# Performance work log

Measured on AMD Instinct MI355X. Metric: run time of the kernel, lower is better.

The kernel has to match this reference:

```python
import jax, jax.numpy as jnp
import numpy as np

N = 8192      # nodes
E = 8192      # target edges
H = 256       # in_channels == hidden_channels (required by module structure)
OUT = 1
ADJ_P = 0.004 # ~33 avg degree


def _linear_params(key, din, dout):
    kw, kb = jax.random.split(key)
    s = 1.0 / np.sqrt(din)
    w = jax.random.uniform(kw, (din, dout), jnp.float32, -s, s)
    b = jax.random.uniform(kb, (dout,), jnp.float32, -s, s)
    return w, b


def setup_inputs() -> dict:
    key = jax.random.key(0)
    ks = jax.random.split(key, 10)
    x = jax.random.normal(ks[0], (N, H), jnp.float32)
    # binary adjacency (symmetric not required by the math)
    adj = (jax.random.uniform(ks[1], (N, N)) < ADJ_P).astype(jnp.float32)
    tar_ei = jax.random.randint(ks[2], (2, E), 0, N)
    xlin_w, xlin_b = _linear_params(ks[3], H, H)
    xcnlin_w, xcnlin_b = _linear_params(ks[4], H, H)
    xijlini_w, xijlini_b = _linear_params(ks[5], H, H)
    xijlinj_w, xijlinj_b = _linear_params(ks[6], H, H)
    xijfinal_w, xijfinal_b = _linear_params(ks[7], H, H)
    xslin_w, xslin_b = _linear_params(ks[8], H, OUT)
    beta = jnp.ones((1,), jnp.float32)
    return {
        'x': x, 'adj': adj, 'tar_ei': tar_ei,
        'xlin_w': xlin_w, 'xlin_b': xlin_b,
        'xcnlin_w': xcnlin_w, 'xcnlin_b': xcnlin_b,
        'xijlini_w': xijlini_w, 'xijlini_b': xijlini_b,
        'xijlinj_w': xijlinj_w, 'xijlinj_b': xijlinj_b,
        'xijfinal_w': xijfinal_w, 'xijfinal_b': xijfinal_b,
        'xslin_w': xslin_w, 'xslin_b': xslin_b,
        'beta': beta, 'boolen': 1,
    }


def reference(x, adj, tar_ei, xlin_w, xlin_b, xcnlin_w, xcnlin_b,
              xijlini_w, xijlini_b, xijlinj_w, xijlinj_b,
              xijfinal_w, xijfinal_b, xslin_w, xslin_b, beta, boolen):
    src, dst = tar_ei[0], tar_ei[1]
    xi = x[src]                       # [E,H]
    xj = x[dst]                       # [E,H]
    x2 = x + (x @ xlin_w + xlin_b)    # x = x + xlin(x)
    # adjoverlap: common-neighbor indicator per target edge = A[i] AND A[j]
    cn = adj[src] * adj[dst]          # [E,N] binary mask
    xcn = cn @ x2                     # spmm_add(cn, x) -> [E,H]
    xij = jax.nn.relu((xi @ xijlini_w + xijlini_b) + (xj @ xijlinj_w + xijlinj_b))
    xij = xij @ xijfinal_w + xijfinal_b
    xs = (xcn @ xcnlin_w + xcnlin_b) * beta + xij
    # NOTE: source's `xs.relu()` result is discarded (not in-place) -> no relu
    xs = xs @ xslin_w + xslin_b       # [E,OUT]
    sign = 1.0 if boolen else -1.0
    return -jax.nn.log_sigmoid(sign * xs)
```

## Files before the change

kernel.cpp:

```cpp
#include <hip/hip_runtime.h>

#define Nn 8192
#define Ee 8192
#define Hh 256
#define MASK_W 128
#define RQ 16
#define NPQ 512

typedef unsigned long long u64;
typedef float nf4 __attribute__((ext_vector_type(4)));

__global__ void __launch_bounds__(256)
pre_kernel(const float* __restrict__ Wc, const float* __restrict__ Wf,
           const float* __restrict__ Wx, const float* __restrict__ v_,
           const float* __restrict__ bc, const float* __restrict__ bf_,
           const float* __restrict__ bx, const float* __restrict__ bs,
           const float* __restrict__ beta, const int* __restrict__ boolen,
           float* __restrict__ w2, float* __restrict__ g,
           float* __restrict__ consts) {
    __shared__ float sv[Hh];
    __shared__ float su[Hh];
    __shared__ float r1[Hh], r2[Hh], r3[Hh];
    const int tid = threadIdx.x;
    sv[tid] = v_[tid];
    __syncthreads();

    const float4* wc4 = reinterpret_cast<const float4*>(Wc + (size_t)tid * Hh);
    const float4* wf4 = reinterpret_cast<const float4*>(Wf + (size_t)tid * Hh);
    const float4* sv4 = reinterpret_cast<const float4*>(sv);
    float a = 0.f, b = 0.f;
#pragma unroll 8
    for (int j = 0; j < Hh / 4; ++j) {
        const float4 w = wc4[j];
        const float4 f = wf4[j];
        const float4 s = sv4[j];
        a = fmaf(w.x, s.x, fmaf(w.y, s.y, fmaf(w.z, s.z, fmaf(w.w, s.w, a))));
        b = fmaf(f.x, s.x, fmaf(f.y, s.y, fmaf(f.z, s.z, fmaf(f.w, s.w, b))));
    }
    su[tid] = a;
    w2[tid] = b;
    __syncthreads();

    const float4* wx4 = reinterpret_cast<const float4*>(Wx + (size_t)tid * Hh);
    const float4* su4 = reinterpret_cast<const float4*>(su);
    float c = a;
#pragma unroll 8
    for (int j = 0; j < Hh / 4; ++j) {
        const float4 w = wx4[j];
        const float4 uu = su4[j];
        c = fmaf(w.x, uu.x, fmaf(w.y, uu.y, fmaf(w.z, uu.z, fmaf(w.w, uu.w, c))));
    }
    g[tid] = c;

    r1[tid] = bc[tid] * sv[tid];
    r2[tid] = bf_[tid] * sv[tid];
    r3[tid] = bx[tid] * a;
    __syncthreads();
    for (int s = 128; s > 0; s >>= 1) {
        if (tid < s) { r1[tid] += r1[tid + s]; r2[tid] += r2[tid + s]; r3[tid] += r3[tid + s]; }
        __syncthreads();
    }
    if (tid == 0) {
        const float be = beta[0];
        consts[0] = r3[0];
        consts[1] = be * r1[0] + r2[0] + bs[0];
        consts[2] = (boolen[0] != 0) ? 1.f : -1.f;
        consts[3] = be;
    }
}

__global__ void __launch_bounds__(256)
fusedA_kernel(const float* __restrict__ adj, u64* __restrict__ mask,
              const float* __restrict__ x,
              const float* __restrict__ Wi, const float* __restrict__ Wj,
              const float* __restrict__ bi, const float* __restrict__ bj,
              const float* __restrict__ g, const float* __restrict__ consts,
              float* __restrict__ P, float* __restrict__ Q,
              float* __restrict__ t) {
    __shared__ float xs[RQ][Hh];
    const int tid = threadIdx.x;

    if (blockIdx.x >= NPQ) {
        const int wave_id = (blockIdx.x - NPQ) * 4 + (tid >> 6);
        const int lane = tid & 63;
        const int row  = wave_id >> 1;
        const int half = wave_id & 1;
        const nf4* src = reinterpret_cast<const nf4*>(
            adj + (size_t)row * Nn + half * 4096);

        u64 myword = 0;
#pragma unroll
        for (int i = 0; i < 16; ++i) {
            const nf4 v = __builtin_nontemporal_load(src + i * 64 + lane);
            unsigned int nib = 0;
            nib |= (v.x != 0.f) ? 1u : 0u;
            nib |= (v.y != 0.f) ? 2u : 0u;
            nib |= (v.z != 0.f) ? 4u : 0u;
            nib |= (v.w != 0.f) ? 8u : 0u;
            const unsigned int t1 = __shfl_xor(nib, 1);
            const unsigned int by = nib | (t1 << 4);
            const unsigned int t2 = __shfl_xor(by, 2);
            const unsigned int h16 = by | (t2 << 8);
            const unsigned int t4 = __shfl_xor(h16, 4);
            const unsigned int w32 = h16 | (t4 << 16);
            const unsigned int t8 = __shfl_xor(w32, 8);
            const u64 w64 = (u64)w32 | ((u64)t8 << 32);
            const u64 got = __shfl(w64, (lane & 3) << 4);
            if ((lane >> 2) == i) myword = got;
        }
        mask[(size_t)row * MASK_W + half * 64 + lane] = myword;
        return;
    }

    const int base = blockIdx.x * RQ;
    {
        const float4* xv = reinterpret_cast<const float4*>(x + (size_t)base * Hh);
        float4* xd = reinterpret_cast<float4*>(&xs[0][0]);
#pragma unroll
        for (int i = tid; i < 1024; i += 256) xd[i] = xv[i];
    }
    __syncthreads();

    {
        const int wave = tid >> 6;
        const int lane = tid & 63;
        const float c0 = consts[0];
#pragma unroll
        for (int r0 = 0; r0 < 4; ++r0) {
            const int r = wave * 4 + r0;
            float s = 0.f;
#pragma unroll
            for (int i = 0; i < 4; ++i) {
                const int c = lane * 4 + i;
                s = fmaf(xs[r][c], g[c], s);
            }
            for (int off = 32; off > 0; off >>= 1) s += __shfl_down(s, off);
            if (lane == 0) t[base + r] = s + c0;
        }
    }

    float accP[RQ], accQ[RQ];
    const float fbi = bi[tid], fbj = bj[tid];
#pragma unroll
    for (int r = 0; r < RQ; ++r) { accP[r] = fbi; accQ[r] = fbj; }

#pragma unroll 4
    for (int k = 0; k < Hh; ++k) {
        const float wiv = Wi[k * Hh + tid];
        const float wjv = Wj[k * Hh + tid];
#pragma unroll
        for (int r = 0; r < RQ; ++r) {
            accP[r] = fmaf(xs[r][k], wiv, accP[r]);
            accQ[r] = fmaf(xs[r][k], wjv, accQ[r]);
        }
    }
#pragma unroll
    for (int r = 0; r < RQ; ++r) {
        P[(size_t)(base + r) * Hh + tid] = accP[r];
        Q[(size_t)(base + r) * Hh + tid] = accQ[r];
    }
}

__global__ void edge_kernel(const u64* __restrict__ mask, const int* __restrict__ tei,
                            const float* __restrict__ P, const float* __restrict__ Q,
                            const float* __restrict__ w2, const float* __restrict__ t,
                            const float* __restrict__ consts, float* __restrict__ out) {
    const int e = blockIdx.x;
    const int tid = threadIdx.x;
    const int src = tei[e];
    const int dst = tei[Ee + e];

    __shared__ u64 ms[MASK_W];
    __shared__ u64 md[MASK_W];
    if (tid < MASK_W) ms[tid] = mask[(size_t)src * MASK_W + tid];
    else              md[tid - MASK_W] = mask[(size_t)dst * MASK_W + (tid - MASK_W)];
    __syncthreads();

    float accA = 0.f;
    if (tid < MASK_W) {
        u64 m = ms[tid] & md[tid];
        while (m) {
            const int b = __builtin_ctzll(m);
            accA += t[tid * 64 + b];
            m &= m - 1;
        }
    }
    const float r = P[(size_t)src * Hh + tid] + Q[(size_t)dst * Hh + tid];
    float accB = (r > 0.f) ? r * w2[tid] : 0.f;

    for (int off = 32; off > 0; off >>= 1) {
        accA += __shfl_down(accA, off);
        accB += __shfl_down(accB, off);
    }
    __shared__ float wA[4], wB[4];
    const int wave = tid >> 6;
    if ((tid & 63) == 0) { wA[wave] = accA; wB[wave] = accB; }
    __syncthreads();
    if (tid == 0) {
        const float sA = wA[0] + wA[1] + wA[2] + wA[3];
        const float sB = wB[0] + wB[1] + wB[2] + wB[3];
        const float be = consts[3];
        const float sgn = consts[2];
        const float s = be * sA + sB + consts[1];
        const float m = -sgn * s;
        const float res = fmaxf(m, 0.f) + log1pf(expf(-fabsf(m)));
        out[e] = res;
    }
}

extern "C" void kernel_launch(void* const* d_in, const int* in_sizes, int n_in,
                              void* d_out, int out_size, void* d_ws, size_t ws_size,
                              hipStream_t stream) {
    const float* x     = (const float*)d_in[0];
    const float* adj   = (const float*)d_in[1];
    const int*   tei   = (const int*)d_in[2];
    const float* Wx    = (const float*)d_in[3];
    const float* bx    = (const float*)d_in[4];
    const float* Wc    = (const float*)d_in[5];
    const float* bc    = (const float*)d_in[6];
    const float* Wi    = (const float*)d_in[7];
    const float* bi    = (const float*)d_in[8];
    const float* Wj    = (const float*)d_in[9];
    const float* bj    = (const float*)d_in[10];
    const float* Wf    = (const float*)d_in[11];
    const float* bf_   = (const float*)d_in[12];
    const float* v_    = (const float*)d_in[13];
    const float* bs    = (const float*)d_in[14];
    const float* beta  = (const float*)d_in[15];
    const int*   booln = (const int*)d_in[16];
    float* out = (float*)d_out;

    float* w2     = (float*)d_ws;
    float* g      = w2 + 256;
    float* consts = g + 256;
    float* t      = consts + 8;
    float* P      = t + 8192;
    float* Q      = P + (size_t)Nn * Hh;
    u64*   mask   = (u64*)(Q + (size_t)Nn * Hh);

    pre_kernel<<<1, 256, 0, stream>>>(Wc, Wf, Wx, v_, bc, bf_, bx, bs, beta,
                                      booln, w2, g, consts);
    fusedA_kernel<<<NPQ + (Nn * 2) / 4, 256, 0, stream>>>(adj, mask, x, Wi, Wj,
                                                          bi, bj, g, consts,
                                                          P, Q, t);
    edge_kernel<<<Ee, 256, 0, stream>>>(mask, tei, P, Q, w2, t, consts, out);
}
```

Baseline: 447.7 us.

## Fold single-block precompute kernel into fusedA by recomputing per block

Removes the separate one-block pre_kernel launch. Each P/Q block of fusedA now recomputes the weight-vector products g and c0 redundantly into shared memory, and block 0 alone writes w2 and consts for the edge kernel. This drops one kernel launch and the serial dependency on a single-block kernel. In exchange, each of the 512 P/Q blocks does two extra 256x256 matrix-vector products, reading Wc and Wx, before its main work.

```diff
diff --git a/kernel.cpp b/kernel.cpp
--- a/kernel.cpp
+++ b/kernel.cpp
@@ -11,73 +11,20 @@
 typedef float nf4 __attribute__((ext_vector_type(4)));
 
 __global__ void __launch_bounds__(256)
-pre_kernel(const float* __restrict__ Wc, const float* __restrict__ Wf,
-           const float* __restrict__ Wx, const float* __restrict__ v_,
-           const float* __restrict__ bc, const float* __restrict__ bf_,
-           const float* __restrict__ bx, const float* __restrict__ bs,
-           const float* __restrict__ beta, const int* __restrict__ boolen,
-           float* __restrict__ w2, float* __restrict__ g,
-           float* __restrict__ consts) {
-    __shared__ float sv[Hh];
-    __shared__ float su[Hh];
-    __shared__ float r1[Hh], r2[Hh], r3[Hh];
-    const int tid = threadIdx.x;
-    sv[tid] = v_[tid];
-    __syncthreads();
-
-    const float4* wc4 = reinterpret_cast<const float4*>(Wc + (size_t)tid * Hh);
-    const float4* wf4 = reinterpret_cast<const float4*>(Wf + (size_t)tid * Hh);
-    const float4* sv4 = reinterpret_cast<const float4*>(sv);
-    float a = 0.f, b = 0.f;
-#pragma unroll 8
-    for (int j = 0; j < Hh / 4; ++j) {
-        const float4 w = wc4[j];
-        const float4 f = wf4[j];
-        const float4 s = sv4[j];
-        a = fmaf(w.x, s.x, fmaf(w.y, s.y, fmaf(w.z, s.z, fmaf(w.w, s.w, a))));
-        b = fmaf(f.x, s.x, fmaf(f.y, s.y, fmaf(f.z, s.z, fmaf(f.w, s.w, b))));
-    }
-    su[tid] = a;
-    w2[tid] = b;
-    __syncthreads();
-
-    const float4* wx4 = reinterpret_cast<const float4*>(Wx + (size_t)tid * Hh);
-    const float4* su4 = reinterpret_cast<const float4*>(su);
-    float c = a;
-#pragma unroll 8
-    for (int j = 0; j < Hh / 4; ++j) {
-        const float4 w = wx4[j];
-        const float4 uu = su4[j];
-        c = fmaf(w.x, uu.x, fmaf(w.y, uu.y, fmaf(w.z, uu.z, fmaf(w.w, uu.w, c))));
-    }
-    g[tid] = c;
-
-    r1[tid] = bc[tid] * sv[tid];
-    r2[tid] = bf_[tid] * sv[tid];
-    r3[tid] = bx[tid] * a;
-    __syncthreads();
-    for (int s = 128; s > 0; s >>= 1) {
-        if (tid < s) { r1[tid] += r1[tid + s]; r2[tid] += r2[tid + s]; r3[tid] += r3[tid + s]; }
-        __syncthreads();
-    }
-    if (tid == 0) {
-        const float be = beta[0];
-        consts[0] = r3[0];
-        consts[1] = be * r1[0] + r2[0] + bs[0];
-        consts[2] = (boolen[0] != 0) ? 1.f : -1.f;
-        consts[3] = be;
-    }
-}
-
-__global__ void __launch_bounds__(256)
 fusedA_kernel(const float* __restrict__ adj, u64* __restrict__ mask,
               const float* __restrict__ x,
               const float* __restrict__ Wi, const float* __restrict__ Wj,
               const float* __restrict__ bi, const float* __restrict__ bj,
-              const float* __restrict__ g, const float* __restrict__ consts,
+              const float* __restrict__ Wc, const float* __restrict__ Wx,
+              const float* __restrict__ Wf, const float* __restrict__ v_,
+              const float* __restrict__ bx, const float* __restrict__ bc,
+              const float* __restrict__ bf_, const float* __restrict__ bs,
+              const float* __restrict__ beta, const int* __restrict__ boolen,
+              float* __restrict__ w2, float* __restrict__ consts,
               float* __restrict__ P, float* __restrict__ Q,
               float* __restrict__ t) {
     __shared__ float xs[RQ][Hh];
+    __shared__ float sg[Hh];
     const int tid = threadIdx.x;
 
     if (blockIdx.x >= NPQ) {
@@ -112,6 +59,75 @@
         return;
     }
 
+    float* sv = xs[0];
+    float* su = xs[1];
+    float* r3 = xs[2];
+    float* r1 = xs[3];
+    float* r2 = xs[4];
+    const bool blk0 = (blockIdx.x == 0);
+
+    sv[tid] = v_[tid];
+    __syncthreads();
+
+    float a = 0.f, b = 0.f;
+    {
+        const float4* wc4 = reinterpret_cast<const float4*>(Wc + (size_t)tid * Hh);
+        const float4* sv4 = reinterpret_cast<const float4*>(sv);
+        if (blk0) {
+            const float4* wf4 = reinterpret_cast<const float4*>(Wf + (size_t)tid * Hh);
+#pragma unroll 8
+            for (int j = 0; j < Hh / 4; ++j) {
+                const float4 w = wc4[j];
+                const float4 f = wf4[j];
+                const float4 s = sv4[j];
+                a = fmaf(w.x, s.x, fmaf(w.y, s.y, fmaf(w.z, s.z, fmaf(w.w, s.w, a))));
+                b = fmaf(f.x, s.x, fmaf(f.y, s.y, fmaf(f.z, s.z, fmaf(f.w, s.w, b))));
+            }
+        } else {
+#pragma unroll 8
+            for (int j = 0; j < Hh / 4; ++j) {
+                const float4 w = wc4[j];
+                const float4 s = sv4[j];
+                a = fmaf(w.x, s.x, fmaf(w.y, s.y, fmaf(w.z, s.z, fmaf(w.w, s.w, a))));
+            }
+        }
+    }
+    su[tid] = a;
+    if (blk0) w2[tid] = b;
+    __syncthreads();
+
+    {
+        const float4* wx4 = reinterpret_cast<const float4*>(Wx + (size_t)tid * Hh);
+        const float4* su4 = reinterpret_cast<const float4*>(su);
+        float c = a;
+#pragma unroll 8
+        for (int j = 0; j < Hh / 4; ++j) {
+            const float4 w = wx4[j];
+            const float4 uu = su4[j];
+            c = fmaf(w.x, uu.x, fmaf(w.y, uu.y, fmaf(w.z, uu.z, fmaf(w.w, uu.w, c))));
+        }
+        sg[tid] = c;
+    }
+
+    r3[tid] = bx[tid] * a;
+    if (blk0) { r1[tid] = bc[tid] * sv[tid]; r2[tid] = bf_[tid] * sv[tid]; }
+    __syncthreads();
+    for (int s = 128; s > 0; s >>= 1) {
+        if (tid < s) {
+            r3[tid] += r3[tid + s];
+            if (blk0) { r1[tid] += r1[tid + s]; r2[tid] += r2[tid + s]; }
+        }
+        __syncthreads();
+    }
+    const float c0 = r3[0];
+    if (blk0 && tid == 0) {
+        const float be = beta[0];
+        consts[1] = be * r1[0] + r2[0] + bs[0];
+        consts[2] = (boolen[0] != 0) ? 1.f : -1.f;
+        consts[3] = be;
+    }
+    __syncthreads();
+
     const int base = blockIdx.x * RQ;
     {
         const float4* xv = reinterpret_cast<const float4*>(x + (size_t)base * Hh);
@@ -124,7 +140,6 @@
     {
         const int wave = tid >> 6;
         const int lane = tid & 63;
-        const float c0 = consts[0];
 #pragma unroll
         for (int r0 = 0; r0 < 4; ++r0) {
             const int r = wave * 4 + r0;
@@ -132,7 +147,7 @@
 #pragma unroll
             for (int i = 0; i < 4; ++i) {
                 const int c = lane * 4 + i;
-                s = fmaf(xs[r][c], g[c], s);
+                s = fmaf(xs[r][c], sg[c], s);
             }
             for (int off = 32; off > 0; off >>= 1) s += __shfl_down(s, off);
             if (lane == 0) t[base + r] = s + c0;
@@ -237,11 +252,10 @@
     float* P      = t + 8192;
     float* Q      = P + (size_t)Nn * Hh;
     u64*   mask   = (u64*)(Q + (size_t)Nn * Hh);
-
-    pre_kernel<<<1, 256, 0, stream>>>(Wc, Wf, Wx, v_, bc, bf_, bx, bs, beta,
-                                      booln, w2, g, consts);
-    fusedA_kernel<<<NPQ + (Nn * 2) / 4, 256, 0, stream>>>(adj, mask, x, Wi, Wj,
-                                                          bi, bj, g, consts,
-                                                          P, Q, t);
+    (void)g;
+
+    fusedA_kernel<<<NPQ + (Nn * 2) / 4, 256, 0, stream>>>(
+        adj, mask, x, Wi, Wj, bi, bj, Wc, Wx, Wf, v_, bx, bc, bf_, bs, beta,
+        booln, w2, consts, P, Q, t);
     edge_kernel<<<Ee, 256, 0, stream>>>(mask, tei, P, Q, w2, t, consts, out);
 }
```

Result: faster. 428.8 us (-4.2%).
